# Optimization experiments

Measured on AMD Instinct MI355X. Metric: run time of the kernel, lower is better.

Reference implementation:

```python
import jax, jax.numpy as jnp
import numpy as np


def _gcn_conv(x, src, dst, norm, W, b, n_nodes):
    # x: [N, Fin] -> [N, Fout]. PyG GCNConv: linear (no bias), normalized
    # scatter-add aggregation over edges (self-loops already in src/dst), + bias.
    h = x @ W                                  # [N, Fout]
    msg = h[src] * norm[:, None]               # [E+N, Fout]
    out = jax.ops.segment_sum(msg, dst, num_segments=n_nodes)
    return out + b


def _prep_edges(edge_index, n_nodes):
    # Add self-loops and compute symmetric normalization deg^-1/2 * deg^-1/2.
    loops = jnp.arange(n_nodes, dtype=edge_index.dtype)
    src = jnp.concatenate([edge_index[0], loops])
    dst = jnp.concatenate([edge_index[1], loops])
    deg = jax.ops.segment_sum(jnp.ones_like(dst, dtype=jnp.float32), dst,
                              num_segments=n_nodes)
    dinv = jnp.where(deg > 0, jax.lax.rsqrt(jnp.maximum(deg, 1.0)), 0.0)
    norm = dinv[src] * dinv[dst]
    return src, dst, norm


def setup_inputs() -> dict:
    key = jax.random.key(0)
    k1, k2, k3, k4 = jax.random.split(key, 4)
    N, Fin, Fout = 50000, 128, 64
    H = 2 * Fout
    E = 640000
    x = jax.random.normal(k1, (N, Fin), dtype=jnp.float32)
    edge_index = jax.random.randint(k2, (2, E), 0, N, dtype=jnp.int64)
    W1 = jax.random.normal(k3, (Fin, H), dtype=jnp.float32) * (1.0 / np.sqrt(Fin))
    b1 = jnp.zeros((H,), dtype=jnp.float32)
    W2 = jax.random.normal(k4, (H, Fout), dtype=jnp.float32) * (1.0 / np.sqrt(H))
    b2 = jnp.zeros((Fout,), dtype=jnp.float32)
    return {"x": x, "edge_index": edge_index, "W1": W1, "b1": b1, "W2": W2, "b2": b2}


def reference(x, edge_index, W1, b1, W2, b2):
    n_nodes = x.shape[0]
    src, dst, norm = _prep_edges(edge_index, n_nodes)
    h = _gcn_conv(x, src, dst, norm, W1, b1, n_nodes)
    h = jax.nn.relu(h)
    return _gcn_conv(h, src, dst, norm, W2, b2, n_nodes)
```

## Files before the change

### kernel.cpp

```cpp
#include <hip/hip_runtime.h>

#define CEILDIV(a,b) (((a)+(b)-1)/(b))

constexpr int CAP = 64;


__device__ __forceinline__ unsigned short f2bf(float f) {
  union { float f; unsigned u; } v; v.f = f;
  unsigned u = v.u + (0x7fffu + ((v.u >> 16) & 1u));
  return (unsigned short)(u >> 16);
}
__device__ __forceinline__ unsigned pack2(float lo, float hi) {
  return (unsigned)f2bf(lo) | ((unsigned)f2bf(hi) << 16);
}
__device__ __forceinline__ void add2(float* a, unsigned w) {
  union { unsigned u; float f; } lo, hi;
  lo.u = w << 16; hi.u = w & 0xffff0000u;
  a[0] += lo.f; a[1] += hi.f;
}
__device__ __forceinline__ void add8(float* a, uint4 w) {
  add2(a + 0, w.x); add2(a + 2, w.y); add2(a + 4, w.z); add2(a + 6, w.w);
}


__global__ __launch_bounds__(256) void k_init(const int* __restrict__ raw,
                                              int* __restrict__ flag,
                                              int* __restrict__ cnt, int N, int E) {
  const int tid = threadIdx.x;
  const int i4 = (blockIdx.x * 256 + tid) * 4;
  if (i4 + 3 < N) {
    *(int4*)&cnt[i4] = make_int4(0, 0, 0, 0);
  } else {
    for (int j = 0; j < 4; ++j)
      if (i4 + j < N) cnt[i4 + j] = 0;
  }
  if (blockIdx.x == 0) {
    __shared__ int ok;
    if (tid == 0) ok = 1;
    __syncthreads();
    int n = (E < 1024) ? E : 1024;
    for (int i = tid; i < n; i += 256)
      if (raw[2 * i + 1] != 0) ok = 0;
    __syncthreads();
    if (tid == 0) *flag = ok;
  }
}

__global__ void k_fill(const int* __restrict__ raw, const int* __restrict__ flag,
                       int* __restrict__ cnt, int* __restrict__ esrc, int E) {
  int e0 = (blockIdx.x * blockDim.x + threadIdx.x) * 4;
  if (e0 >= E) return;
  const bool is64 = (*flag != 0);
  if (((E & 3) == 0) && e0 + 3 < E) {
    int s[4], d[4];
    if (is64) {
      uint4 sa = *(const uint4*)&raw[2 * e0];
      uint4 sb = *(const uint4*)&raw[2 * e0 + 4];
      uint4 da = *(const uint4*)&raw[2 * (E + e0)];
      uint4 db = *(const uint4*)&raw[2 * (E + e0) + 4];
      s[0] = (int)sa.x; s[1] = (int)sa.z; s[2] = (int)sb.x; s[3] = (int)sb.z;
      d[0] = (int)da.x; d[1] = (int)da.z; d[2] = (int)db.x; d[3] = (int)db.z;
    } else {
      uint4 sv = *(const uint4*)&raw[e0];
      uint4 dv = *(const uint4*)&raw[E + e0];
      s[0] = (int)sv.x; s[1] = (int)sv.y; s[2] = (int)sv.z; s[3] = (int)sv.w;
      d[0] = (int)dv.x; d[1] = (int)dv.y; d[2] = (int)dv.z; d[3] = (int)dv.w;
    }
    int p[4];
#pragma unroll
    for (int j = 0; j < 4; ++j) p[j] = atomicAdd(&cnt[d[j]], 1);
#pragma unroll
    for (int j = 0; j < 4; ++j)
      if (p[j] < CAP) esrc[(size_t)d[j] * CAP + p[j]] = s[j];
  } else {
    for (int e = e0; e < E && e < e0 + 4; ++e) {
      int s = is64 ? raw[2 * e] : raw[e];
      int d = is64 ? raw[2 * (E + e)] : raw[E + e];
      int pos = atomicAdd(&cnt[d], 1);
      if (pos < CAP) esrc[(size_t)d * CAP + pos] = s;
    }
  }
}

template <int K, int NO>
__global__ __launch_bounds__(256, 2) void k_gemm(const float* __restrict__ X,
                                                 const float* __restrict__ W,
                                                 const int* __restrict__ cnt,
                                                 unsigned short* __restrict__ Y,
                                                 int N) {
  constexpr int ROWS = 128, KC = 64, TC = NO / 16;
  constexpr int XST = ROWS + 4;
  constexpr int WST = NO + 4;
  __shared__ float xs[KC * XST];
  __shared__ float ws[KC * WST];
  const int tid = threadIdx.x;
  const int tx = tid & 15, ty = tid >> 4;
  const int c0 = tx * TC, r0 = ty * 8;
  const int row0 = blockIdx.x * ROWS;

  float acc[8][TC];
#pragma unroll
  for (int i = 0; i < 8; ++i)
#pragma unroll
    for (int j = 0; j < TC; ++j) acc[i][j] = 0.0f;

  for (int kk = 0; kk < K; kk += KC) {
#pragma unroll
    for (int it = 0; it < (ROWS * KC / 4) / 256; ++it) {
      int idx = it * 256 + tid;
      int r = idx >> 4, kq = idx & 15;
      int row = row0 + r; if (row >= N) row = N - 1;
      float4 v = *(const float4*)&X[(size_t)row * K + kk + kq * 4];
      xs[(kq * 4 + 0) * XST + r] = v.x;
      xs[(kq * 4 + 1) * XST + r] = v.y;
      xs[(kq * 4 + 2) * XST + r] = v.z;
      xs[(kq * 4 + 3) * XST + r] = v.w;
    }
#pragma unroll
    for (int it = 0; it < (KC * NO / 4) / 256; ++it) {
      int idx = it * 256 + tid;
      int c4 = idx & (NO / 4 - 1), kw = idx / (NO / 4);
      float4 v = *(const float4*)&W[(size_t)(kk + kw) * NO + c4 * 4];
      *(float4*)&ws[kw * WST + c4 * 4] = v;
    }
    __syncthreads();
#pragma unroll 4
    for (int k = 0; k < KC; ++k) {
      const float4 xa = *(const float4*)&xs[k * XST + r0];
      const float4 xb = *(const float4*)&xs[k * XST + r0 + 4];
      float4 wv[TC / 4];
#pragma unroll
      for (int j4 = 0; j4 < TC / 4; ++j4)
        wv[j4] = *(const float4*)&ws[k * WST + c0 + j4 * 4];
      const float xr[8] = {xa.x, xa.y, xa.z, xa.w, xb.x, xb.y, xb.z, xb.w};
#pragma unroll
      for (int i = 0; i < 8; ++i)
#pragma unroll
        for (int j4 = 0; j4 < TC / 4; ++j4) {
          acc[i][j4 * 4 + 0] += xr[i] * wv[j4].x;
          acc[i][j4 * 4 + 1] += xr[i] * wv[j4].y;
          acc[i][j4 * 4 + 2] += xr[i] * wv[j4].z;
          acc[i][j4 * 4 + 3] += xr[i] * wv[j4].w;
        }
    }
    __syncthreads();
  }
#pragma unroll
  for (int i = 0; i < 8; ++i) {
    int r = row0 + r0 + i;
    if (r < N) {
      float dv = rsqrtf((float)(cnt[r] + 1));
      unsigned pk[TC / 2];
#pragma unroll
      for (int j = 0; j < TC / 2; ++j)
        pk[j] = pack2(acc[i][2 * j] * dv, acc[i][2 * j + 1] * dv);
      if constexpr (TC == 8) {
        *(uint4*)&Y[(size_t)r * NO + c0] = make_uint4(pk[0], pk[1], pk[2], pk[3]);
      } else {
        *(uint2*)&Y[(size_t)r * NO + c0] = make_uint2(pk[0], pk[1]);
      }
    }
  }
}

template <int F, bool RELU>
__global__ __launch_bounds__(256) void k_agg(const unsigned short* __restrict__ h,
                                             const int* __restrict__ cnt,
                                             const int* __restrict__ esrc,
                                             const float* __restrict__ bias,
                                             float* __restrict__ out, int N) {
  constexpr int LPN = F / 8;
  constexpr int NPB = 256 / LPN;
  const int v = blockIdx.x * NPB + threadIdx.x / LPN;
  if (v >= N) return;
  const int lc = threadIdx.x % LPN;
  const uint4* __restrict__ h4 = (const uint4*)h;

  float acc[8] = {0, 0, 0, 0, 0, 0, 0, 0};
  add8(acc, h4[(size_t)v * LPN + lc]);
  const int deg = min(cnt[v], CAP);
  const float dv = rsqrtf((float)(deg + 1));
  const int* __restrict__ ep = &esrc[(size_t)v * CAP];
  int e = 0;
  for (; e + 4 <= deg; e += 4) {
    int s0 = ep[e + 0], s1 = ep[e + 1], s2 = ep[e + 2], s3 = ep[e + 3];
    uint4 a0 = h4[(size_t)s0 * LPN + lc];
    uint4 a1 = h4[(size_t)s1 * LPN + lc];
    uint4 a2 = h4[(size_t)s2 * LPN + lc];
    uint4 a3 = h4[(size_t)s3 * LPN + lc];
    add8(acc, a0); add8(acc, a1); add8(acc, a2); add8(acc, a3);
  }
  for (; e < deg; ++e) add8(acc, h4[(size_t)ep[e] * LPN + lc]);

  const float4 b0 = *(const float4*)&bias[lc * 8];
  const float4 b1 = *(const float4*)&bias[lc * 8 + 4];
  float4 o0, o1;
  o0.x = acc[0] * dv + b0.x; o0.y = acc[1] * dv + b0.y;
  o0.z = acc[2] * dv + b0.z; o0.w = acc[3] * dv + b0.w;
  o1.x = acc[4] * dv + b1.x; o1.y = acc[5] * dv + b1.y;
  o1.z = acc[6] * dv + b1.z; o1.w = acc[7] * dv + b1.w;
  if (RELU) {
    o0.x = fmaxf(o0.x, 0.0f); o0.y = fmaxf(o0.y, 0.0f);
    o0.z = fmaxf(o0.z, 0.0f); o0.w = fmaxf(o0.w, 0.0f);
    o1.x = fmaxf(o1.x, 0.0f); o1.y = fmaxf(o1.y, 0.0f);
    o1.z = fmaxf(o1.z, 0.0f); o1.w = fmaxf(o1.w, 0.0f);
  }
  float4* op = (float4*)(out + (size_t)v * F + lc * 8);
  op[0] = o0; op[1] = o1;
}


extern "C" void kernel_launch(void* const* d_in, const int* in_sizes, int n_in,
                              void* d_out, int out_size, void* d_ws, size_t ws_size,
                              hipStream_t stream) {
  const float* x  = (const float*)d_in[0];
  const int*   ei = (const int*)d_in[1];
  const float* W1 = (const float*)d_in[2];
  const float* b1 = (const float*)d_in[3];
  const float* W2 = (const float*)d_in[4];
  const float* b2 = (const float*)d_in[5];
  const int H    = in_sizes[3];
  const int Fin  = in_sizes[2] / H;
  const int N    = in_sizes[0] / Fin;
  const int E    = in_sizes[1] / 2;
  const int FO   = in_sizes[5];
  float* outp = (float*)d_out;

  char* p = (char*)d_ws;
  auto alloc = [&](size_t bytes) {
    void* q = (void*)p;
    p += (bytes + 255) & ~(size_t)255;
    return q;
  };
  int*   flag = (int*)alloc(256);
  int*   cnt  = (int*)alloc((size_t)N * 4);
  int*   esrc = (int*)alloc((size_t)N * CAP * 4);
  unsigned short* hb1 = (unsigned short*)alloc((size_t)N * H * 2);
  unsigned short* hb2 = (unsigned short*)alloc((size_t)N * FO * 2);
  float* a1   = (float*)alloc((size_t)N * H * 4);

  const int NB = CEILDIV(N, 1024);
  k_init<<<NB, 256, 0, stream>>>(ei, flag, cnt, N, E);
  k_fill<<<CEILDIV(E, 1024), 256, 0, stream>>>(ei, flag, cnt, esrc, E);

  k_gemm<128, 128><<<CEILDIV(N, 128), 256, 0, stream>>>(x, W1, cnt, hb1, N);
  k_agg<128, true><<<CEILDIV(N, 16), 256, 0, stream>>>(hb1, cnt, esrc, b1, a1, N);

  k_gemm<128, 64><<<CEILDIV(N, 128), 256, 0, stream>>>(a1, W2, cnt, hb2, N);
  k_agg<64, false><<<CEILDIV(N, 32), 256, 0, stream>>>(hb2, cnt, esrc, b2, outp, N);
}
```

Before: 141.2 us.

## Fuse edge fill with first GEMM and store layer-1 activations in bf16

Merges the edge-bucketing kernel and the first GEMM into one launch with interleaved block roles, so the scatter atomics overlap the dense matmul. Because the GEMM now runs before degrees are known, source-side normalization moves into the first aggregation, which does an extra per-edge load of the neighbor count and an rsqrt. Layer-1 activations are written as bf16 instead of fp32, halving that intermediate traffic, and the second GEMM converts them on load. The degree scaling also now uses the uncapped count instead of the count clamped at CAP.

```diff
diff --git a/kernel.cpp b/kernel.cpp
--- a/kernel.cpp
+++ b/kernel.cpp
@@ -20,6 +20,14 @@
 }
 __device__ __forceinline__ void add8(float* a, uint4 w) {
   add2(a + 0, w.x); add2(a + 2, w.y); add2(a + 4, w.z); add2(a + 6, w.w);
+}
+__device__ __forceinline__ void fma2(float* a, unsigned w, float s) {
+  union { unsigned u; float f; } lo, hi;
+  lo.u = w << 16; hi.u = w & 0xffff0000u;
+  a[0] = fmaf(lo.f, s, a[0]); a[1] = fmaf(hi.f, s, a[1]);
+}
+__device__ __forceinline__ void fma8(float* a, uint4 w, float s) {
+  fma2(a + 0, w.x, s); fma2(a + 2, w.y, s); fma2(a + 4, w.z, s); fma2(a + 6, w.w, s);
 }
 
 
@@ -46,9 +54,120 @@
   }
 }
 
-__global__ void k_fill(const int* __restrict__ raw, const int* __restrict__ flag,
-                       int* __restrict__ cnt, int* __restrict__ esrc, int E) {
-  int e0 = (blockIdx.x * blockDim.x + threadIdx.x) * 4;
+template <int K, int NO, bool XBF16, bool SCALE>
+__device__ __forceinline__ void gemm_body(const void* __restrict__ Xv,
+                                          const float* __restrict__ W,
+                                          const int* __restrict__ cnt,
+                                          unsigned short* __restrict__ Y,
+                                          int N, int bid) {
+  constexpr int ROWS = 128, KC = 64, TC = NO / 16;
+  constexpr int XST = ROWS + 4;
+  constexpr int WST = NO + 4;
+  __shared__ float xs[KC * XST];
+  __shared__ float ws[KC * WST];
+  const int tid = threadIdx.x;
+  const int tx = tid & 15, ty = tid >> 4;
+  const int c0 = tx * TC, r0 = ty * 8;
+  const int row0 = bid * ROWS;
+
+  float acc[8][TC];
+#pragma unroll
+  for (int i = 0; i < 8; ++i)
+#pragma unroll
+    for (int j = 0; j < TC; ++j) acc[i][j] = 0.0f;
+
+  for (int kk = 0; kk < K; kk += KC) {
+#pragma unroll
+    for (int it = 0; it < (ROWS * KC / 4) / 256; ++it) {
+      int idx = it * 256 + tid;
+      int r = idx >> 4, kq = idx & 15;
+      int row = row0 + r; if (row >= N) row = N - 1;
+      float f0, f1, f2, f3;
+      if constexpr (XBF16) {
+        const unsigned short* Xb = (const unsigned short*)Xv;
+        uint2 v = *(const uint2*)&Xb[(size_t)row * K + kk + kq * 4];
+        union { unsigned u; float f; } t0, t1, t2, t3;
+        t0.u = v.x << 16; t1.u = v.x & 0xffff0000u;
+        t2.u = v.y << 16; t3.u = v.y & 0xffff0000u;
+        f0 = t0.f; f1 = t1.f; f2 = t2.f; f3 = t3.f;
+      } else {
+        const float* Xf = (const float*)Xv;
+        float4 v = *(const float4*)&Xf[(size_t)row * K + kk + kq * 4];
+        f0 = v.x; f1 = v.y; f2 = v.z; f3 = v.w;
+      }
+      xs[(kq * 4 + 0) * XST + r] = f0;
+      xs[(kq * 4 + 1) * XST + r] = f1;
+      xs[(kq * 4 + 2) * XST + r] = f2;
+      xs[(kq * 4 + 3) * XST + r] = f3;
+    }
+#pragma unroll
+    for (int it = 0; it < (KC * NO / 4) / 256; ++it) {
+      int idx = it * 256 + tid;
+      int c4 = idx & (NO / 4 - 1), kw = idx / (NO / 4);
+      float4 v = *(const float4*)&W[(size_t)(kk + kw) * NO + c4 * 4];
+      *(float4*)&ws[kw * WST + c4 * 4] = v;
+    }
+    __syncthreads();
+#pragma unroll 4
+    for (int k = 0; k < KC; ++k) {
+      const float4 xa = *(const float4*)&xs[k * XST + r0];
+      const float4 xb = *(const float4*)&xs[k * XST + r0 + 4];
+      float4 wv[TC / 4];
+#pragma unroll
+      for (int j4 = 0; j4 < TC / 4; ++j4)
+        wv[j4] = *(const float4*)&ws[k * WST + c0 + j4 * 4];
+      const float xr[8] = {xa.x, xa.y, xa.z, xa.w, xb.x, xb.y, xb.z, xb.w};
+#pragma unroll
+      for (int i = 0; i < 8; ++i)
+#pragma unroll
+        for (int j4 = 0; j4 < TC / 4; ++j4) {
+          acc[i][j4 * 4 + 0] += xr[i] * wv[j4].x;
+          acc[i][j4 * 4 + 1] += xr[i] * wv[j4].y;
+          acc[i][j4 * 4 + 2] += xr[i] * wv[j4].z;
+          acc[i][j4 * 4 + 3] += xr[i] * wv[j4].w;
+        }
+    }
+    __syncthreads();
+  }
+#pragma unroll
+  for (int i = 0; i < 8; ++i) {
+    int r = row0 + r0 + i;
+    if (r < N) {
+      float dv = SCALE ? rsqrtf((float)(cnt[r] + 1)) : 1.0f;
+      unsigned pk[TC / 2];
+#pragma unroll
+      for (int j = 0; j < TC / 2; ++j)
+        pk[j] = pack2(acc[i][2 * j] * dv, acc[i][2 * j + 1] * dv);
+      if constexpr (TC == 8) {
+        *(uint4*)&Y[(size_t)r * NO + c0] = make_uint4(pk[0], pk[1], pk[2], pk[3]);
+      } else {
+        *(uint2*)&Y[(size_t)r * NO + c0] = make_uint2(pk[0], pk[1]);
+      }
+    }
+  }
+}
+
+__global__ __launch_bounds__(256, 2) void k_fused(
+    const float* __restrict__ X, const float* __restrict__ W1,
+    unsigned short* __restrict__ hb1, int N, int GB,
+    const int* __restrict__ raw, const int* __restrict__ flag,
+    int* __restrict__ cnt, int* __restrict__ esrc, int E, int FB) {
+  const int i = blockIdx.x;
+  const int m = (FB < GB) ? FB : GB;
+  int fid = -1, gid = -1;
+  if (i < 2 * m) {
+    if ((i & 1) == 0) fid = i >> 1; else gid = i >> 1;
+  } else {
+    int r = i - 2 * m;
+    if (FB > GB) fid = m + r; else gid = m + r;
+  }
+
+  if (gid >= 0) {
+    gemm_body<128, 128, false, false>(X, W1, nullptr, hb1, N, gid);
+    return;
+  }
+
+  int e0 = (fid * 256 + threadIdx.x) * 4;
   if (e0 >= E) return;
   const bool is64 = (*flag != 0);
   if (((E & 3) == 0) && e0 + 3 < E) {
@@ -82,93 +201,71 @@
   }
 }
 
-template <int K, int NO>
-__global__ __launch_bounds__(256, 2) void k_gemm(const float* __restrict__ X,
-                                                 const float* __restrict__ W,
-                                                 const int* __restrict__ cnt,
-                                                 unsigned short* __restrict__ Y,
-                                                 int N) {
-  constexpr int ROWS = 128, KC = 64, TC = NO / 16;
-  constexpr int XST = ROWS + 4;
-  constexpr int WST = NO + 4;
-  __shared__ float xs[KC * XST];
-  __shared__ float ws[KC * WST];
-  const int tid = threadIdx.x;
-  const int tx = tid & 15, ty = tid >> 4;
-  const int c0 = tx * TC, r0 = ty * 8;
-  const int row0 = blockIdx.x * ROWS;
-
-  float acc[8][TC];
-#pragma unroll
-  for (int i = 0; i < 8; ++i)
-#pragma unroll
-    for (int j = 0; j < TC; ++j) acc[i][j] = 0.0f;
-
-  for (int kk = 0; kk < K; kk += KC) {
-#pragma unroll
-    for (int it = 0; it < (ROWS * KC / 4) / 256; ++it) {
-      int idx = it * 256 + tid;
-      int r = idx >> 4, kq = idx & 15;
-      int row = row0 + r; if (row >= N) row = N - 1;
-      float4 v = *(const float4*)&X[(size_t)row * K + kk + kq * 4];
-      xs[(kq * 4 + 0) * XST + r] = v.x;
-      xs[(kq * 4 + 1) * XST + r] = v.y;
-      xs[(kq * 4 + 2) * XST + r] = v.z;
-      xs[(kq * 4 + 3) * XST + r] = v.w;
-    }
-#pragma unroll
-    for (int it = 0; it < (KC * NO / 4) / 256; ++it) {
-      int idx = it * 256 + tid;
-      int c4 = idx & (NO / 4 - 1), kw = idx / (NO / 4);
-      float4 v = *(const float4*)&W[(size_t)(kk + kw) * NO + c4 * 4];
-      *(float4*)&ws[kw * WST + c4 * 4] = v;
-    }
-    __syncthreads();
-#pragma unroll 4
-    for (int k = 0; k < KC; ++k) {
-      const float4 xa = *(const float4*)&xs[k * XST + r0];
-      const float4 xb = *(const float4*)&xs[k * XST + r0 + 4];
-      float4 wv[TC / 4];
-#pragma unroll
-      for (int j4 = 0; j4 < TC / 4; ++j4)
-        wv[j4] = *(const float4*)&ws[k * WST + c0 + j4 * 4];
-      const float xr[8] = {xa.x, xa.y, xa.z, xa.w, xb.x, xb.y, xb.z, xb.w};
-#pragma unroll
-      for (int i = 0; i < 8; ++i)
-#pragma unroll
-        for (int j4 = 0; j4 < TC / 4; ++j4) {
-          acc[i][j4 * 4 + 0] += xr[i] * wv[j4].x;
-          acc[i][j4 * 4 + 1] += xr[i] * wv[j4].y;
-          acc[i][j4 * 4 + 2] += xr[i] * wv[j4].z;
-          acc[i][j4 * 4 + 3] += xr[i] * wv[j4].w;
-        }
-    }
-    __syncthreads();
-  }
-#pragma unroll
-  for (int i = 0; i < 8; ++i) {
-    int r = row0 + r0 + i;
-    if (r < N) {
-      float dv = rsqrtf((float)(cnt[r] + 1));
-      unsigned pk[TC / 2];
-#pragma unroll
-      for (int j = 0; j < TC / 2; ++j)
-        pk[j] = pack2(acc[i][2 * j] * dv, acc[i][2 * j + 1] * dv);
-      if constexpr (TC == 8) {
-        *(uint4*)&Y[(size_t)r * NO + c0] = make_uint4(pk[0], pk[1], pk[2], pk[3]);
-      } else {
-        *(uint2*)&Y[(size_t)r * NO + c0] = make_uint2(pk[0], pk[1]);
-      }
-    }
-  }
-}
-
-template <int F, bool RELU>
-__global__ __launch_bounds__(256) void k_agg(const unsigned short* __restrict__ h,
-                                             const int* __restrict__ cnt,
-                                             const int* __restrict__ esrc,
-                                             const float* __restrict__ bias,
-                                             float* __restrict__ out, int N) {
+__global__ __launch_bounds__(256) void k_agg1(const unsigned short* __restrict__ h,
+                                              const int* __restrict__ cnt,
+                                              const int* __restrict__ esrc,
+                                              const float* __restrict__ bias,
+                                              unsigned short* __restrict__ out,
+                                              int N) {
+  const int v = blockIdx.x * 16 + (threadIdx.x >> 4);
+  if (v >= N) return;
+  const int lc = threadIdx.x & 15;
+  const uint4* __restrict__ h4 = (const uint4*)h;
+
+  const int cv = cnt[v];
+  const int deg = min(cv, CAP);
+  const float dv = rsqrtf((float)(cv + 1));
+  float acc[8] = {0, 0, 0, 0, 0, 0, 0, 0};
+  fma8(acc, h4[(size_t)v * 16 + lc], dv);
+  const int* __restrict__ ep = &esrc[(size_t)v * CAP];
+  int e = 0;
+  for (; e + 4 <= deg; e += 4) {
+    int s0 = ep[e + 0], s1 = ep[e + 1], s2 = ep[e + 2], s3 = ep[e + 3];
+    float w0 = rsqrtf((float)(cnt[s0] + 1));
+    float w1 = rsqrtf((float)(cnt[s1] + 1));
+    float w2 = rsqrtf((float)(cnt[s2] + 1));
+    float w3 = rsqrtf((float)(cnt[s3] + 1));
+    uint4 a0 = h4[(size_t)s0 * 16 + lc];
+    uint4 a1 = h4[(size_t)s1 * 16 + lc];
+    uint4 a2 = h4[(size_t)s2 * 16 + lc];
+    uint4 a3 = h4[(size_t)s3 * 16 + lc];
+    fma8(acc, a0, w0); fma8(acc, a1, w1); fma8(acc, a2, w2); fma8(acc, a3, w3);
+  }
+  for (; e < deg; ++e) {
+    int s = ep[e];
+    fma8(acc, h4[(size_t)s * 16 + lc], rsqrtf((float)(cnt[s] + 1)));
+  }
+
+  const float4 b0 = *(const float4*)&bias[lc * 8];
+  const float4 b1 = *(const float4*)&bias[lc * 8 + 4];
+  float r[8];
+  r[0] = fmaxf(acc[0] * dv + b0.x, 0.0f);
+  r[1] = fmaxf(acc[1] * dv + b0.y, 0.0f);
+  r[2] = fmaxf(acc[2] * dv + b0.z, 0.0f);
+  r[3] = fmaxf(acc[3] * dv + b0.w, 0.0f);
+  r[4] = fmaxf(acc[4] * dv + b1.x, 0.0f);
+  r[5] = fmaxf(acc[5] * dv + b1.y, 0.0f);
+  r[6] = fmaxf(acc[6] * dv + b1.z, 0.0f);
+  r[7] = fmaxf(acc[7] * dv + b1.w, 0.0f);
+  uint4 pk = make_uint4(pack2(r[0], r[1]), pack2(r[2], r[3]),
+                        pack2(r[4], r[5]), pack2(r[6], r[7]));
+  ((uint4*)out)[(size_t)v * 16 + lc] = pk;
+}
+
+__global__ __launch_bounds__(256, 2) void k_gemm2(const unsigned short* __restrict__ X,
+                                                  const float* __restrict__ W,
+                                                  const int* __restrict__ cnt,
+                                                  unsigned short* __restrict__ Y,
+                                                  int N) {
+  gemm_body<128, 64, true, true>(X, W, cnt, Y, N, blockIdx.x);
+}
+
+template <int F>
+__global__ __launch_bounds__(256) void k_agg2(const unsigned short* __restrict__ h,
+                                              const int* __restrict__ cnt,
+                                              const int* __restrict__ esrc,
+                                              const float* __restrict__ bias,
+                                              float* __restrict__ out, int N) {
   constexpr int LPN = F / 8;
   constexpr int NPB = 256 / LPN;
   const int v = blockIdx.x * NPB + threadIdx.x / LPN;
@@ -178,8 +275,9 @@
 
   float acc[8] = {0, 0, 0, 0, 0, 0, 0, 0};
   add8(acc, h4[(size_t)v * LPN + lc]);
-  const int deg = min(cnt[v], CAP);
-  const float dv = rsqrtf((float)(deg + 1));
+  const int cv = cnt[v];
+  const int deg = min(cv, CAP);
+  const float dv = rsqrtf((float)(cv + 1));
   const int* __restrict__ ep = &esrc[(size_t)v * CAP];
   int e = 0;
   for (; e + 4 <= deg; e += 4) {
@@ -199,12 +297,6 @@
   o0.z = acc[2] * dv + b0.z; o0.w = acc[3] * dv + b0.w;
   o1.x = acc[4] * dv + b1.x; o1.y = acc[5] * dv + b1.y;
   o1.z = acc[6] * dv + b1.z; o1.w = acc[7] * dv + b1.w;
-  if (RELU) {
-    o0.x = fmaxf(o0.x, 0.0f); o0.y = fmaxf(o0.y, 0.0f);
-    o0.z = fmaxf(o0.z, 0.0f); o0.w = fmaxf(o0.w, 0.0f);
-    o1.x = fmaxf(o1.x, 0.0f); o1.y = fmaxf(o1.y, 0.0f);
-    o1.z = fmaxf(o1.z, 0.0f); o1.w = fmaxf(o1.w, 0.0f);
-  }
   float4* op = (float4*)(out + (size_t)v * F + lc * 8);
   op[0] = o0; op[1] = o1;
 }
@@ -236,16 +328,16 @@
   int*   cnt  = (int*)alloc((size_t)N * 4);
   int*   esrc = (int*)alloc((size_t)N * CAP * 4);
   unsigned short* hb1 = (unsigned short*)alloc((size_t)N * H * 2);
+  unsigned short* ab1 = (unsigned short*)alloc((size_t)N * H * 2);
   unsigned short* hb2 = (unsigned short*)alloc((size_t)N * FO * 2);
-  float* a1   = (float*)alloc((size_t)N * H * 4);
 
   const int NB = CEILDIV(N, 1024);
+  const int FB = CEILDIV(E, 1024);
+  const int GB = CEILDIV(N, 128);
+
   k_init<<<NB, 256, 0, stream>>>(ei, flag, cnt, N, E);
-  k_fill<<<CEILDIV(E, 1024), 256, 0, stream>>>(ei, flag, cnt, esrc, E);
-
-  k_gemm<128, 128><<<CEILDIV(N, 128), 256, 0, stream>>>(x, W1, cnt, hb1, N);
-  k_agg<128, true><<<CEILDIV(N, 16), 256, 0, stream>>>(hb1, cnt, esrc, b1, a1, N);
-
-  k_gemm<128, 64><<<CEILDIV(N, 128), 256, 0, stream>>>(a1, W2, cnt, hb2, N);
-  k_agg<64, false><<<CEILDIV(N, 32), 256, 0, stream>>>(hb2, cnt, esrc, b2, outp, N);
-}
+  k_fused<<<FB + GB, 256, 0, stream>>>(x, W1, hb1, N, GB, ei, flag, cnt, esrc, E, FB);
+  k_agg1<<<CEILDIV(N, 16), 256, 0, stream>>>(hb1, cnt, esrc, b1, ab1, N);
+  k_gemm2<<<CEILDIV(N, 128), 256, 0, stream>>>(ab1, W2, cnt, hb2, N);
+  k_agg2<64><<<CEILDIV(N, 32), 256, 0, stream>>>(hb2, cnt, esrc, b2, outp, N);
+}
```

Result: faster. 129.6 us (-8.2%).
